# Optimization experiments

Hardware: AMD Instinct MI355X
Metric: run time of the kernel (lower is better)

The kernel has to match this reference:

```python
import jax, jax.numpy as jnp
import numpy as np

B, T, D = 2, 2048, 1024
H = 16
DH = D // H
SCALE = DH ** -0.5


def setup_inputs() -> dict:
    key = jax.random.key(0)
    ks = jax.random.split(key, 9)
    s = D ** -0.5
    return {
        "x": jax.random.normal(ks[0], (B, T, D), dtype=jnp.float32),
        "Wq": jax.random.normal(ks[1], (D, D), dtype=jnp.float32) * s,
        "bq": jax.random.normal(ks[2], (D,), dtype=jnp.float32) * 0.01,
        "Wk": jax.random.normal(ks[3], (D, D), dtype=jnp.float32) * s,
        "bk": jax.random.normal(ks[4], (D,), dtype=jnp.float32) * 0.01,
        "Wv": jax.random.normal(ks[5], (D, D), dtype=jnp.float32) * s,
        "bv": jax.random.normal(ks[6], (D,), dtype=jnp.float32) * 0.01,
        "Wo": jax.random.normal(ks[7], (D, D), dtype=jnp.float32) * s,
        "bo": jax.random.normal(ks[8], (D,), dtype=jnp.float32) * 0.01,
    }


def reference(x, Wq, bq, Wk, bk, Wv, bv, Wo, bo):
    # projections; torch Linear: y = x @ W.T + b. Here W is stored as (in, out).
    q = (x @ Wq + bq).reshape(B, T, H, DH).transpose(0, 2, 1, 3)  # (B,H,T,DH)
    k = (x @ Wk + bk).reshape(B, T, H, DH).transpose(0, 2, 1, 3)
    v = (x @ Wv + bv).reshape(B, T, H, DH).transpose(0, 2, 1, 3)
    scores = jnp.einsum("bhqd,bhkd->bhqk", q, k) * SCALE  # (B,H,T,T)
    causal = jnp.tril(jnp.ones((T, T), dtype=bool))
    scores = jnp.where(causal, scores, -jnp.inf)
    probs = jax.nn.softmax(scores, axis=-1)
    out = jnp.einsum("bhqk,bhkd->bhqd", probs, v)  # (B,H,T,DH)
    out = out.transpose(0, 2, 1, 3).reshape(B, T, D)
    out = out @ Wo + bo
    return out, (k, v)
```

## Files before the change

kernel.cpp:

```cpp
#include <hip/hip_runtime.h>

typedef float  f32x4  __attribute__((ext_vector_type(4)));
typedef float  f32x16 __attribute__((ext_vector_type(16)));
typedef __bf16 bf16x8 __attribute__((ext_vector_type(8)));
typedef short  s16x8  __attribute__((ext_vector_type(8)));
typedef short  s16x4  __attribute__((ext_vector_type(4)));
typedef unsigned int u32x4 __attribute__((ext_vector_type(4)));

static __device__ __forceinline__ unsigned short f2bf(float f) {
  return __builtin_bit_cast(unsigned short, (__bf16)f);
}
static __device__ __forceinline__ bf16x8 bc8(s16x8 v) {
  return __builtin_bit_cast(bf16x8, v);
}
static __device__ __forceinline__ f32x16 mfma32(bf16x8 a, bf16x8 b, f32x16 c) {
  return __builtin_amdgcn_mfma_f32_32x32x16_bf16(a, b, c, 0, 0, 0);
}
static __device__ __forceinline__ f32x4 mfma16(bf16x8 a, bf16x8 b, f32x4 c) {
  return __builtin_amdgcn_mfma_f32_16x16x32_bf16(a, b, c, 0, 0, 0);
}

static __device__ __forceinline__ void gl2lds16(const unsigned short* g, unsigned short* l) {
  __builtin_amdgcn_global_load_lds(
      (const __attribute__((address_space(1))) unsigned int*)g,
      (__attribute__((address_space(3))) unsigned int*)l, 16, 0, 0);
}

#define GSYNC(NSTR)                                          \
  do {                                                       \
    __builtin_amdgcn_sched_barrier(0);                       \
    asm volatile("s_waitcnt vmcnt(" NSTR ")" ::: "memory");  \
    __builtin_amdgcn_s_barrier();                            \
    __builtin_amdgcn_sched_barrier(0);                       \
  } while (0)

__global__ void prep_k(const float* __restrict__ x, unsigned short* __restrict__ xb,
                       const float* __restrict__ W0, const float* __restrict__ W1,
                       const float* __restrict__ W2, const float* __restrict__ W3,
                       unsigned short* __restrict__ wtb) {
  __shared__ unsigned short tl[64][72];
  const int bid = blockIdx.x;
  const int t = threadIdx.x;
  if (bid < 2048) {
    int i = (bid * 256 + t) * 8;
    float4 a = *(const float4*)(x + i);
    float4 b = *(const float4*)(x + i + 4);
    s16x8 o;
    o[0] = (short)f2bf(a.x); o[1] = (short)f2bf(a.y);
    o[2] = (short)f2bf(a.z); o[3] = (short)f2bf(a.w);
    o[4] = (short)f2bf(b.x); o[5] = (short)f2bf(b.y);
    o[6] = (short)f2bf(b.z); o[7] = (short)f2bf(b.w);
    *(s16x8*)(xb + i) = o;
    return;
  }
  const int rid = bid - 2048;
  const int z = rid >> 8, rem = rid & 255;
  const float* W = z == 0 ? W0 : z == 1 ? W1 : z == 2 ? W2 : W3;
  unsigned short* out = wtb + (size_t)z * 1048576;
  const int nt = (rem & 15) * 64, kt = (rem >> 4) * 64;
  const int row = t >> 2, seg = t & 3;
  const float* src = W + (kt + row) * 1024 + nt + seg * 16;
#pragma unroll
  for (int q = 0; q < 4; ++q) {
    float4 v = *(const float4*)(src + q * 4);
    tl[seg * 16 + q * 4 + 0][row] = f2bf(v.x);
    tl[seg * 16 + q * 4 + 1][row] = f2bf(v.y);
    tl[seg * 16 + q * 4 + 2][row] = f2bf(v.z);
    tl[seg * 16 + q * 4 + 3][row] = f2bf(v.w);
  }
  __syncthreads();
  unsigned short* dst = out + (nt + row) * 1024 + kt + seg * 16;
  *(s16x8*)dst       = *(const s16x8*)&tl[row][seg * 16];
  *(s16x8*)(dst + 8) = *(const s16x8*)&tl[row][seg * 16 + 8];
}

static __device__ __forceinline__ int trans_ix(int m, int n) {
  int b = m >> 11, tt = m & 2047, h = n >> 6, dh = n & 63;
  return ((b << 4) + h) * 131072 + tt * 64 + dh;
}

__global__ __launch_bounds__(512, 4) void gemm_qkv_k(const unsigned short* __restrict__ A,
                                                     const unsigned short* __restrict__ BT,
                                                     const float* __restrict__ b0,
                                                     const float* __restrict__ b1,
                                                     const float* __restrict__ b2,
                                                     float* __restrict__ outF,
                                                     unsigned short* __restrict__ oq,
                                                     unsigned short* __restrict__ ok,
                                                     unsigned short* __restrict__ ovT) {
  extern __shared__ unsigned short lds[];
  const int t = threadIdx.x;
  const int lane = t & 63, ln = lane & 15, g = lane >> 4;
  const int w = t >> 6, wm = w >> 2, wn = w & 3;
  const unsigned wgid = blockIdx.x;
  const int xcd = wgid & 7;
  const int loc = wgid >> 3;
  const int by = (xcd & 3) * 8 + (loc & 7);
  const int bx = (xcd >> 2) * 8 + (loc >> 3);
  const int bm0 = by * 128, bn0 = bx * 192;

  const int ar = t >> 2;
  const unsigned short* aBase = A + (size_t)(bm0 + ar) * 1024 + (((t & 3) ^ ((ar >> 1) & 3)) * 8);
  const int br = t >> 3;
  const int bcol = (t & 7) ^ (br & 7);
  const unsigned short* bBase = BT + (size_t)(bn0 + br) * 1024 + bcol * 8;

  auto issueA = [&](int buf, int H, int kt) {
    gl2lds16(aBase + kt + H * 32, &lds[buf * 20480 + H * 4096 + t * 8]);
  };
  auto issueB = [&](int buf, int j, int kt) {
    gl2lds16(bBase + (size_t)j * 65536 + kt, &lds[buf * 20480 + 8192 + j * 4096 + t * 8]);
  };
  auto ldA = [&](int buf, int H, int mf) -> bf16x8 {
    const int row = wm * 64 + mf * 16 + ln;
    const int sp = g ^ ((row >> 1) & 3);
    return bc8(*(const s16x8*)&lds[buf * 20480 + H * 4096 + row * 32 + sp * 8]);
  };
  auto ldB = [&](int buf, int H, int nf) -> bf16x8 {
    const int row = wn * 48 + nf * 16 + ln;
    const int sp = (H * 4 + g) ^ (row & 7);
    return bc8(*(const s16x8*)&lds[buf * 20480 + 8192 + row * 64 + sp * 8]);
  };

  f32x4 acc[4][3] = {};
  issueA(0, 0, 0);
  issueB(0, 0, 0);
  issueB(0, 1, 0);
  issueB(0, 2, 0);
  issueA(0, 1, 0);

  for (int ti = 0; ti < 16; ++ti) {
    const int buf = ti & 1, nb = buf ^ 1;
    const bool hn = ti < 15;
    const int kn = (ti + 1) * 64;

    GSYNC("1");
    if (hn) { issueA(nb, 0, kn); issueB(nb, 0, kn); issueB(nb, 1, kn); }
    {
      bf16x8 afr[4], bfr[3];
#pragma unroll
      for (int mf = 0; mf < 4; ++mf) afr[mf] = ldA(buf, 0, mf);
#pragma unroll
      for (int nf = 0; nf < 3; ++nf) bfr[nf] = ldB(buf, 0, nf);
      __builtin_amdgcn_s_setprio(1);
#pragma unroll
      for (int mf = 0; mf < 4; ++mf)
#pragma unroll
        for (int nf = 0; nf < 3; ++nf) acc[mf][nf] = mfma16(afr[mf], bfr[nf], acc[mf][nf]);
      __builtin_amdgcn_s_setprio(0);
    }
    if (hn) GSYNC("3"); else GSYNC("0");
    if (hn) { issueB(nb, 2, kn); issueA(nb, 1, kn); }
    {
      bf16x8 afr[4], bfr[3];
#pragma unroll
      for (int mf = 0; mf < 4; ++mf) afr[mf] = ldA(buf, 1, mf);
#pragma unroll
      for (int nf = 0; nf < 3; ++nf) bfr[nf] = ldB(buf, 1, nf);
      __builtin_amdgcn_s_setprio(1);
#pragma unroll
      for (int mf = 0; mf < 4; ++mf)
#pragma unroll
        for (int nf = 0; nf < 3; ++nf) acc[mf][nf] = mfma16(afr[mf], bfr[nf], acc[mf][nf]);
      __builtin_amdgcn_s_setprio(0);
    }
  }

#pragma unroll
  for (int nf = 0; nf < 3; ++nf) {
    const int n = bn0 + wn * 48 + nf * 16 + ln;
    const int n1 = n & 1023;
    const float* bp = n < 1024 ? b0 : (n < 2048 ? b1 : b2);
    const float bias = bp[n1];
    if (n < 1024) {
#pragma unroll
      for (int mf = 0; mf < 4; ++mf)
#pragma unroll
        for (int r = 0; r < 4; ++r) {
          const int m = bm0 + wm * 64 + mf * 16 + g * 4 + r;
          oq[trans_ix(m, n1)] = f2bf((acc[mf][nf][r] + bias) * 0.18033688f);
        }
    } else if (n < 2048) {
#pragma unroll
      for (int mf = 0; mf < 4; ++mf)
#pragma unroll
        for (int r = 0; r < 4; ++r) {
          const int m = bm0 + wm * 64 + mf * 16 + g * 4 + r;
          const float v = acc[mf][nf][r] + bias;
          const int ix = trans_ix(m, n1);
          ok[ix] = f2bf(v);
          outF[4194304 + ix] = v;
        }
    } else {
      const int dh = n1 & 63, hh = n1 >> 6;
#pragma unroll
      for (int mf = 0; mf < 4; ++mf) {
        const int m0 = bm0 + wm * 64 + mf * 16 + g * 4;
        const int bb = m0 >> 11, tt = m0 & 2047;
        s16x4 pv;
#pragma unroll
        for (int r = 0; r < 4; ++r) {
          const float v = acc[mf][nf][r] + bias;
          outF[8388608 + trans_ix(m0 + r, n1)] = v;
          pv[r] = (short)f2bf(v);
        }
        *(s16x4*)(ovT + (size_t)((bb << 4) + hh) * 131072 + (size_t)dh * 2048 + tt) = pv;
      }
    }
  }
}

__global__ __launch_bounds__(512, 4) void gemm_o_k(const unsigned short* __restrict__ A,
                                                   const unsigned short* __restrict__ BT,
                                                   const float* __restrict__ b0,
                                                   float* __restrict__ outF) {
  extern __shared__ unsigned short lds[];
  const int t = threadIdx.x;
  const int lane = t & 63, ln = lane & 15, g = lane >> 4;
  const int w = t >> 6, wm = w >> 2, wn = w & 3;
  const unsigned wgid = blockIdx.x;
  const unsigned swz = (wgid & 7) * 64 + (wgid >> 3);
  const int bx = swz & 7, by = swz >> 3;
  const int bm0 = by * 64, bn0 = bx * 128;

  const int row = t >> 3;
  const int scol = (t & 7) ^ (row & 7);
  const unsigned short* aSrc = A + (size_t)(bm0 + row) * 1024 + scol * 8;
  const unsigned short* bSrc0 = BT + (size_t)(bn0 + row) * 1024 + scol * 8;
  const unsigned short* bSrc1 = BT + (size_t)(bn0 + 64 + row) * 1024 + scol * 8;

  auto issue3 = [&](int buf, int ti) {
    const int kt = ti * 64;
    gl2lds16(aSrc + kt, &lds[buf * 12288 + t * 8]);
    gl2lds16(bSrc0 + kt, &lds[buf * 12288 + 4096 + t * 8]);
    gl2lds16(bSrc1 + kt, &lds[buf * 12288 + 8192 + t * 8]);
  };
  auto ldA = [&](int buf, int H, int mf) -> bf16x8 {
    const int r = wm * 32 + mf * 16 + ln;
    const int sp = (H * 4 + g) ^ (r & 7);
    return bc8(*(const s16x8*)&lds[buf * 12288 + r * 64 + sp * 8]);
  };
  auto ldB = [&](int buf, int H, int nf) -> bf16x8 {
    const int r = wn * 32 + nf * 16 + ln;
    const int j = r >> 6, rl = r & 63;
    const int sp = (H * 4 + g) ^ (rl & 7);
    return bc8(*(const s16x8*)&lds[buf * 12288 + 4096 + j * 4096 + rl * 64 + sp * 8]);
  };

  f32x4 acc[2][2] = {};
  issue3(0, 0);
  issue3(1, 1);

  for (int i = 0; i < 16; ++i) {
    const int buf = i & 1;
    if (i < 15) GSYNC("3"); else GSYNC("0");
    bf16x8 a0[2], a1[2], bq0[2], bq1[2];
#pragma unroll
    for (int mf = 0; mf < 2; ++mf) { a0[mf] = ldA(buf, 0, mf); a1[mf] = ldA(buf, 1, mf); }
#pragma unroll
    for (int nf = 0; nf < 2; ++nf) { bq0[nf] = ldB(buf, 0, nf); bq1[nf] = ldB(buf, 1, nf); }
    asm volatile("s_waitcnt lgkmcnt(0)" ::: "memory");
    __builtin_amdgcn_sched_barrier(0);
    __builtin_amdgcn_s_barrier();
    __builtin_amdgcn_sched_barrier(0);
    if (i + 2 < 16) issue3(buf, i + 2);
    __builtin_amdgcn_s_setprio(1);
#pragma unroll
    for (int mf = 0; mf < 2; ++mf)
#pragma unroll
      for (int nf = 0; nf < 2; ++nf) {
        acc[mf][nf] = mfma16(a0[mf], bq0[nf], acc[mf][nf]);
        acc[mf][nf] = mfma16(a1[mf], bq1[nf], acc[mf][nf]);
      }
    __builtin_amdgcn_s_setprio(0);
  }

#pragma unroll
  for (int nf = 0; nf < 2; ++nf) {
    const int n = bn0 + wn * 32 + nf * 16 + ln;
    const float bias = b0[n];
#pragma unroll
    for (int mf = 0; mf < 2; ++mf)
#pragma unroll
      for (int r = 0; r < 4; ++r) {
        const int m = bm0 + wm * 32 + mf * 16 + g * 4 + r;
        outF[(size_t)m * 1024 + n] = acc[mf][nf][r] + bias;
      }
  }
}

__global__ __launch_bounds__(768) void attn_k(const unsigned short* __restrict__ qb,
                                              const unsigned short* __restrict__ kb,
                                              const unsigned short* __restrict__ vbT,
                                              unsigned short* __restrict__ ob) {
  extern __shared__ s16x8 kvS[];
  const int t = threadIdx.x;
  const int lane = t & 63, l31 = lane & 31, h5 = lane >> 5;
  const int w = t >> 6, grp = w >> 2, qw = w & 3;
  const unsigned wg = blockIdx.x;
  const int x = wg & 7, r_ = wg >> 3;
  const int bh = x + 8 * (r_ >> 3);
  const int p = r_ & 7;
  const int b = bh >> 4, h = bh & 15;
  const unsigned short* Qp = qb + (size_t)bh * 131072;
  const unsigned short* Kp = kb + (size_t)bh * 131072;
  const unsigned short* Vp = vbT + (size_t)bh * 131072;

  const int e0 = t & 255;
  const int kr0 = e0 >> 3;
  const int kcol = (e0 & 7) ^ (kr0 & 7);
  const unsigned short* kSrc = Kp + (size_t)kr0 * 64 + kcol * 8;
  const unsigned short* vSrc = Vp + (size_t)kr0 * 2048 + kcol * 8;
  s16x8* gB = &kvS[grp * 3072];

  s16x8 onesv;
#pragma unroll
  for (int z = 0; z < 8; ++z) onesv[z] = (short)0x3F80;
  const bf16x8 onesf = bc8(onesv);

  float* sc = (float*)kvS;
  const int slot = qw * 64 + lane;

  for (int half = 0; half < 2; ++half) {
    const int qblk = half == 0 ? p : 15 - p;
    const int q0 = qblk * 128;
    const int N64 = 2 * qblk + 2;
    const int base = N64 / 3, rem3 = N64 % 3;
    const int cnt = base + (grp < rem3 ? 1 : 0);
    const int start = grp * base + (grp < rem3 ? grp : rem3);
    const int NP = base + (rem3 ? 1 : 0);
    const int qg = q0 + qw * 32 + l31;

    __syncthreads();

    bf16x8 qf[4];
#pragma unroll
    for (int m = 0; m < 4; ++m)
      qf[m] = bc8(*(const s16x8*)(Qp + (size_t)qg * 64 + 16 * m + 8 * h5));

    auto issue = [&](int T, int buf) {
      const int kv0 = T * 64;
      unsigned short* kd = (unsigned short*)&gB[buf * 1024];
      unsigned short* vd = (unsigned short*)&gB[buf * 1024 + 512];
      const unsigned short* ks = kSrc + (size_t)kv0 * 64;
      const unsigned short* vs = vSrc + kv0;
      gl2lds16(ks,         kd + e0 * 8);
      gl2lds16(ks + 2048,  kd + (e0 + 256) * 8);
      gl2lds16(vs,         vd + e0 * 8);
      gl2lds16(vs + 65536, vd + (e0 + 256) * 8);
    };

    if (cnt > 0) issue(start, 0);
    if (cnt > 1) issue(start + 1, 1);

    f32x16 o0 = {}, o1 = {}, lsum = {};

    for (int i = 0; i < NP; ++i) {
      __builtin_amdgcn_sched_barrier(0);
      if (i + 1 < cnt) asm volatile("s_waitcnt vmcnt(4)" ::: "memory");
      else             asm volatile("s_waitcnt vmcnt(0)" ::: "memory");
      __builtin_amdgcn_s_barrier();
      __builtin_amdgcn_sched_barrier(0);
      if (i + 2 < cnt) issue(start + i + 2, (i + 2) % 3);
      const int T = start + i;
      const int kv0 = T * 64;
      const bool active = (i < cnt) && (kv0 <= q0 + qw * 32 + 31);
      if (active) {
        const int buf = i % 3;
        const s16x8* kb_ = &gB[buf * 1024];
        const s16x8* vb2 = &gB[buf * 1024 + 512];
        f32x16 s0 = {}, s1 = {};
        __builtin_amdgcn_s_setprio(1);
#pragma unroll
        for (int m = 0; m < 4; ++m) {
          const int sl = 2 * m + h5;
          bf16x8 a0 = bc8(kb_[l31 * 8 + (sl ^ (l31 & 7))]);
          bf16x8 a1 = bc8(kb_[(l31 + 32) * 8 + (sl ^ (l31 & 7))]);
          s0 = mfma32(a0, qf[m], s0);
          s1 = mfma32(a1, qf[m], s1);
        }
        __builtin_amdgcn_s_setprio(0);
        if (kv0 + 63 > q0 + qw * 32) {
#pragma unroll
          for (int r = 0; r < 16; ++r) {
            const int kvr = kv0 + (r & 3) + 8 * (r >> 2) + 4 * h5;
            if (kvr > qg) s0[r] = -1e30f;
            if (kvr + 32 > qg) s1[r] = -1e30f;
          }
        }
#pragma unroll
        for (int r = 0; r < 16; ++r) {
          s0[r] = __builtin_amdgcn_exp2f(s0[r]);
          s1[r] = __builtin_amdgcn_exp2f(s1[r]);
        }
        unsigned og[2][4][2];
#pragma unroll
        for (int gg = 0; gg < 4; ++gg) {
          asm("v_cvt_pk_bf16_f32 %0, %1, %2" : "=v"(og[0][gg][0]) : "v"(s0[4 * gg]),     "v"(s0[4 * gg + 1]));
          asm("v_cvt_pk_bf16_f32 %0, %1, %2" : "=v"(og[0][gg][1]) : "v"(s0[4 * gg + 2]), "v"(s0[4 * gg + 3]));
          asm("v_cvt_pk_bf16_f32 %0, %1, %2" : "=v"(og[1][gg][0]) : "v"(s1[4 * gg]),     "v"(s1[4 * gg + 1]));
          asm("v_cvt_pk_bf16_f32 %0, %1, %2" : "=v"(og[1][gg][1]) : "v"(s1[4 * gg + 2]), "v"(s1[4 * gg + 3]));
        }
        bf16x8 pf[4];
#pragma unroll
        for (int mp = 0; mp < 4; ++mp) {
          const int tau = mp >> 1, lc = mp & 1;
          unsigned a0 = og[tau][2 * lc][0], bq0 = og[tau][2 * lc + 1][0];
          unsigned a1 = og[tau][2 * lc][1], bq1 = og[tau][2 * lc + 1][1];
          asm volatile("v_permlane32_swap_b32 %0, %1" : "+v"(a0), "+v"(bq0));
          asm volatile("v_permlane32_swap_b32 %0, %1" : "+v"(a1), "+v"(bq1));
          u32x4 fw; fw[0] = a0; fw[1] = a1; fw[2] = bq0; fw[3] = bq1;
          pf[mp] = __builtin_bit_cast(bf16x8, fw);
        }
        __builtin_amdgcn_s_setprio(1);
#pragma unroll
        for (int mp = 0; mp < 4; ++mp) {
          const int sl = 2 * mp + h5;
          bf16x8 va0 = bc8(vb2[l31 * 8 + (sl ^ (l31 & 7))]);
          bf16x8 va1 = bc8(vb2[(l31 + 32) * 8 + (sl ^ (l31 & 7))]);
          o0 = mfma32(va0, pf[mp], o0);
          o1 = mfma32(va1, pf[mp], o1);
          lsum = mfma32(onesf, pf[mp], lsum);
        }
        __builtin_amdgcn_s_setprio(0);
      }
    }

    __syncthreads();
    if (grp > 0) {
      float* dst = sc + (size_t)(grp - 1) * 8704 + (size_t)slot * 34;
#pragma unroll
      for (int r = 0; r < 8; ++r) {
        *(float2*)(dst + 2 * r)      = make_float2(o0[2 * r], o0[2 * r + 1]);
        *(float2*)(dst + 16 + 2 * r) = make_float2(o1[2 * r], o1[2 * r + 1]);
      }
      dst[32] = lsum[0];
    }
    __syncthreads();
    if (grp == 0) {
      const float* p0 = sc + (size_t)slot * 34;
      const float* p1 = p0 + 8704;
      const float inv = 1.0f / (lsum[0] + p0[32] + p1[32]);
      unsigned short* orow = ob + (size_t)(b * 2048 + qg) * 1024 + h * 64;
#pragma unroll
      for (int rq = 0; rq < 4; ++rq) {
        s16x4 ov0, ov1;
#pragma unroll
        for (int e = 0; e < 4; ++e) {
          const int ei = 4 * rq + e;
          ov0[e] = (short)f2bf((o0[ei] + p0[ei] + p1[ei]) * inv);
          ov1[e] = (short)f2bf((o1[ei] + p0[16 + ei] + p1[16 + ei]) * inv);
        }
        *(s16x4*)(orow + 8 * rq + 4 * h5)      = ov0;
        *(s16x4*)(orow + 32 + 8 * rq + 4 * h5) = ov1;
      }
    }
  }
}

extern "C" void kernel_launch(void* const* d_in, const int* in_sizes, int n_in,
                              void* d_out, int out_size, void* d_ws, size_t ws_size,
                              hipStream_t stream) {
  (void)in_sizes; (void)n_in; (void)out_size; (void)ws_size;
  const float* x  = (const float*)d_in[0];
  const float* Wq = (const float*)d_in[1];
  const float* bq = (const float*)d_in[2];
  const float* Wk = (const float*)d_in[3];
  const float* bk = (const float*)d_in[4];
  const float* Wv = (const float*)d_in[5];
  const float* bv = (const float*)d_in[6];
  const float* Wo = (const float*)d_in[7];
  const float* bo = (const float*)d_in[8];
  float* out = (float*)d_out;

  unsigned short* ws  = (unsigned short*)d_ws;
  unsigned short* xb  = ws;
  unsigned short* wtb = ws + 4194304;
  unsigned short* qbuf = ws + 8388608;
  unsigned short* kbuf = qbuf + 4194304;
  unsigned short* vbuf = kbuf + 4194304;
  unsigned short* ab   = vbuf + 4194304;

  prep_k<<<3072, 256, 0, stream>>>(x, xb, Wq, Wk, Wv, Wo, wtb);
  gemm_qkv_k<<<512, 512, 81920, stream>>>(xb, wtb, bq, bk, bv, out, qbuf, kbuf, vbuf);
  attn_k<<<256, 768, 147456, stream>>>(qbuf, kbuf, vbuf, ab);
  gemm_o_k<<<512, 512, 49152, stream>>>(ab, wtb + 3145728, bo, out);
}
```

Measured before the change: 92.77 us.

## Restructure QKV GEMM pipeline to prefetch two tiles ahead with single barrier

Reworks the QKV projection GEMM main loop so each iteration loads both K-halves of fragments from LDS up front, runs the first half of MFMAs, then barriers once and issues the global-to-LDS load for tile ti+2 into the just-freed buffer before the second half of MFMAs. This replaces the previous scheme of two syncs per iteration with loads one tile ahead. The aim is deeper overlap of global loads with compute and fewer barriers. The cost is more live fragment registers and tighter reliance on hand-set waitcnt values, which must match the load counts exactly.

```diff
diff --git a/kernel.cpp b/kernel.cpp
--- a/kernel.cpp
+++ b/kernel.cpp
@@ -105,11 +105,13 @@
   const int bcol = (t & 7) ^ (br & 7);
   const unsigned short* bBase = BT + (size_t)(bn0 + br) * 1024 + bcol * 8;
 
-  auto issueA = [&](int buf, int H, int kt) {
-    gl2lds16(aBase + kt + H * 32, &lds[buf * 20480 + H * 4096 + t * 8]);
-  };
-  auto issueB = [&](int buf, int j, int kt) {
-    gl2lds16(bBase + (size_t)j * 65536 + kt, &lds[buf * 20480 + 8192 + j * 4096 + t * 8]);
+  auto issueTile = [&](int T, int buf) {
+    const int kt = T * 64;
+    gl2lds16(aBase + kt, &lds[buf * 20480 + t * 8]);
+#pragma unroll
+    for (int j = 0; j < 3; ++j)
+      gl2lds16(bBase + (size_t)j * 65536 + kt, &lds[buf * 20480 + 8192 + j * 4096 + t * 8]);
+    gl2lds16(aBase + kt + 32, &lds[buf * 20480 + 4096 + t * 8]);
   };
   auto ldA = [&](int buf, int H, int mf) -> bf16x8 {
     const int row = wm * 64 + mf * 16 + ln;
@@ -123,47 +125,44 @@
   };
 
   f32x4 acc[4][3] = {};
-  issueA(0, 0, 0);
-  issueB(0, 0, 0);
-  issueB(0, 1, 0);
-  issueB(0, 2, 0);
-  issueA(0, 1, 0);
+  issueTile(0, 0);
+  issueTile(1, 1);
 
   for (int ti = 0; ti < 16; ++ti) {
-    const int buf = ti & 1, nb = buf ^ 1;
-    const bool hn = ti < 15;
-    const int kn = (ti + 1) * 64;
-
-    GSYNC("1");
-    if (hn) { issueA(nb, 0, kn); issueB(nb, 0, kn); issueB(nb, 1, kn); }
-    {
-      bf16x8 afr[4], bfr[3];
-#pragma unroll
-      for (int mf = 0; mf < 4; ++mf) afr[mf] = ldA(buf, 0, mf);
-#pragma unroll
-      for (int nf = 0; nf < 3; ++nf) bfr[nf] = ldB(buf, 0, nf);
-      __builtin_amdgcn_s_setprio(1);
-#pragma unroll
-      for (int mf = 0; mf < 4; ++mf)
-#pragma unroll
-        for (int nf = 0; nf < 3; ++nf) acc[mf][nf] = mfma16(afr[mf], bfr[nf], acc[mf][nf]);
-      __builtin_amdgcn_s_setprio(0);
-    }
-    if (hn) GSYNC("3"); else GSYNC("0");
-    if (hn) { issueB(nb, 2, kn); issueA(nb, 1, kn); }
-    {
-      bf16x8 afr[4], bfr[3];
-#pragma unroll
-      for (int mf = 0; mf < 4; ++mf) afr[mf] = ldA(buf, 1, mf);
-#pragma unroll
-      for (int nf = 0; nf < 3; ++nf) bfr[nf] = ldB(buf, 1, nf);
-      __builtin_amdgcn_s_setprio(1);
-#pragma unroll
-      for (int mf = 0; mf < 4; ++mf)
-#pragma unroll
-        for (int nf = 0; nf < 3; ++nf) acc[mf][nf] = mfma16(afr[mf], bfr[nf], acc[mf][nf]);
-      __builtin_amdgcn_s_setprio(0);
-    }
+    const int buf = ti & 1;
+    if (ti < 15) GSYNC("5"); else GSYNC("0");
+
+    bf16x8 af0[4], bf0[3], af1[4], bf1[3];
+#pragma unroll
+    for (int mf = 0; mf < 4; ++mf) af0[mf] = ldA(buf, 0, mf);
+#pragma unroll
+    for (int nf = 0; nf < 3; ++nf) bf0[nf] = ldB(buf, 0, nf);
+#pragma unroll
+    for (int mf = 0; mf < 4; ++mf) af1[mf] = ldA(buf, 1, mf);
+#pragma unroll
+    for (int nf = 0; nf < 3; ++nf) bf1[nf] = ldB(buf, 1, nf);
+
+    asm volatile("s_waitcnt lgkmcnt(7)" ::: "memory");
+    __builtin_amdgcn_sched_barrier(0);
+    __builtin_amdgcn_s_setprio(1);
+#pragma unroll
+    for (int mf = 0; mf < 4; ++mf)
+#pragma unroll
+      for (int nf = 0; nf < 3; ++nf) acc[mf][nf] = mfma16(af0[mf], bf0[nf], acc[mf][nf]);
+    __builtin_amdgcn_s_setprio(0);
+
+    asm volatile("s_waitcnt lgkmcnt(0)" ::: "memory");
+    __builtin_amdgcn_sched_barrier(0);
+    __builtin_amdgcn_s_barrier();
+    __builtin_amdgcn_sched_barrier(0);
+    if (ti + 2 < 16) issueTile(ti + 2, buf);
+
+    __builtin_amdgcn_s_setprio(1);
+#pragma unroll
+    for (int mf = 0; mf < 4; ++mf)
+#pragma unroll
+      for (int nf = 0; nf < 3; ++nf) acc[mf][nf] = mfma16(af1[mf], bf1[nf], acc[mf][nf]);
+    __builtin_amdgcn_s_setprio(0);
   }
 
 #pragma unroll
```

Measured after the change: 91.83 us, median of 2. About the same (-1.0%).
